# Performance work log

Hardware: AMD Instinct MI355X
Metric: run time of the kernel (lower is better)

Reference implementation:

```python
import jax, jax.numpy as jnp
import numpy as np

HIDDEN = 256


def _lstm_cell(x, h, c, W_ih, W_hh, b_ih, b_hh):
    # torch.nn.LSTMCell: gates ordered [i, f, g, o], gates = x W_ih^T + h W_hh^T + b_ih + b_hh
    gates = x @ W_ih.T + h @ W_hh.T + (b_ih + b_hh)
    i, f, g, o = jnp.split(gates, 4, axis=-1)
    c_new = jax.nn.sigmoid(f) * c + jax.nn.sigmoid(i) * jnp.tanh(g)
    h_new = jax.nn.sigmoid(o) * jnp.tanh(c_new)
    return h_new, c_new


def setup_inputs() -> dict:
    key = jax.random.key(0)
    ks = jax.random.split(key, 16)
    s = 1.0 / np.sqrt(HIDDEN)  # torch LSTMCell init scale
    inp = {
        "tracks": jax.random.normal(ks[0], (256, 512, 2), dtype=jnp.float32),
        "W_ih0": jax.random.uniform(ks[1], (1024, 2), jnp.float32, -s, s),
        "W_hh0": jax.random.uniform(ks[2], (1024, 256), jnp.float32, -s, s),
        "b_ih0": jax.random.uniform(ks[3], (1024,), jnp.float32, -s, s),
        "b_hh0": jax.random.uniform(ks[4], (1024,), jnp.float32, -s, s),
        "W_ih1": jax.random.uniform(ks[5], (1024, 256), jnp.float32, -s, s),
        "W_hh1": jax.random.uniform(ks[6], (1024, 256), jnp.float32, -s, s),
        "b_ih1": jax.random.uniform(ks[7], (1024,), jnp.float32, -s, s),
        "b_hh1": jax.random.uniform(ks[8], (1024,), jnp.float32, -s, s),
        "W_ih2": jax.random.uniform(ks[9], (1024, 256), jnp.float32, -s, s),
        "W_hh2": jax.random.uniform(ks[10], (1024, 256), jnp.float32, -s, s),
        "b_ih2": jax.random.uniform(ks[11], (1024,), jnp.float32, -s, s),
        "b_hh2": jax.random.uniform(ks[12], (1024,), jnp.float32, -s, s),
        "W_pred": jax.random.uniform(ks[13], (2, 256), jnp.float32, -s, s),
        "b_pred": jax.random.uniform(ks[14], (2,), jnp.float32, -s, s),
    }
    return inp


def reference(tracks, W_ih0, W_hh0, b_ih0, b_hh0, W_ih1, W_hh1, b_ih1, b_hh1,
              W_ih2, W_hh2, b_ih2, b_hh2, W_pred, b_pred):
    B = tracks.shape[0]
    layers = [(W_ih0, W_hh0, b_ih0, b_hh0),
              (W_ih1, W_hh1, b_ih1, b_hh1),
              (W_ih2, W_hh2, b_ih2, b_hh2)]
    zeros = jnp.zeros((B, HIDDEN), dtype=tracks.dtype)
    init_carry = tuple((zeros, zeros) for _ in layers)

    def step(carry, x_t):
        new_carry = []
        h = x_t
        for (hc, params) in zip(carry, layers):
            h, c = _lstm_cell(h, hc[0], hc[1], *params)
            new_carry.append((h, c))
        return tuple(new_carry), None

    xs = jnp.swapaxes(tracks, 0, 1)  # [T, B, 2]
    final_carry, _ = jax.lax.scan(step, init_carry, xs)
    h = final_carry[-1][0]  # last layer's final hidden state
    h = jax.nn.elu(h)
    return h @ W_pred.T + b_pred
```

## Files before the change

### kernel.cpp

```cpp
#include <hip/hip_runtime.h>
#include <math.h>

typedef __attribute__((ext_vector_type(4))) float f32x4;
typedef __attribute__((ext_vector_type(4))) int   i32x4;
typedef __attribute__((ext_vector_type(8))) short bfrag8;

#define WRE_LO_OFF 2621440
#define HB_OFF     5242880
#define FA_OFF     6029312
#define FF_OFF     6078464
#define WS_END     6127616

#define WROW 264
#define SMEM_BYTES (4 * 64 * WROW * 2)

__device__ __forceinline__ unsigned short f2bf(float f){
  union { float f; unsigned u; } x; x.f = f;
  unsigned r = x.u + 0x7FFFu + ((x.u >> 16) & 1u);
  return (unsigned short)(r >> 16);
}
__device__ __forceinline__ float bf2f(unsigned short s){
  union { unsigned u; float f; } x; x.u = ((unsigned)s) << 16; return x.f;
}
__device__ __forceinline__ float sigf(float x){
  return 1.0f / (1.0f + __expf(-x));
}
__device__ __forceinline__ float tanh_fast(float x){
  x = fminf(fmaxf(x, -15.0f), 15.0f);
  float e = __expf(2.0f * x);
  return (e - 1.0f) / (e + 1.0f);
}

__device__ __forceinline__ i32x4 llc_load_b128(const void* p){
  i32x4 r;
  asm volatile("global_load_dwordx4 %0, %1, off sc0 sc1"
               : "=v"(r) : "v"(p) : "memory");
  return r;
}
__device__ __forceinline__ void llc_store_b16(void* p, unsigned short v){
  unsigned int vv = v;
  asm volatile("global_store_short %0, %1, off sc0 sc1"
               : : "v"(p), "v"(vv) : "memory");
}
__device__ __forceinline__ void llc_store_u32(void* p, unsigned v){
  asm volatile("global_store_dword %0, %1, off sc0 sc1"
               : : "v"(p), "v"(v) : "memory");
}
__device__ __forceinline__ unsigned poll_llc(const unsigned int* p){
  unsigned r;
  asm volatile("global_load_dword %0, %1, off sc0 sc1\n\ts_waitcnt vmcnt(0)"
               : "=v"(r) : "v"(p) : "memory");
  return r;
}
__device__ __forceinline__ void wait_vm0(){
  asm volatile("s_waitcnt vmcnt(0)" ::: "memory");
}

__global__ void init_reorder(const float* __restrict__ hh0, const float* __restrict__ ih1,
                             const float* __restrict__ hh1, const float* __restrict__ ih2,
                             const float* __restrict__ hh2,
                             unsigned short* __restrict__ wre_hi,
                             unsigned short* __restrict__ wre_lo){
  int e = blockIdx.x * 256 + threadIdx.x;
  int mat = e >> 18;
  int d   = (e >> 8) & 1023;
  int k   = e & 255;
  int nt = d >> 6, g = (d >> 4) & 3, n = d & 15;
  int src_row = g*256 + nt*16 + n;
  const float* W = (mat==0) ? hh0 : (mat==1) ? ih1 : (mat==2) ? hh1 : (mat==3) ? ih2 : hh2;
  float v = W[src_row*256 + k];
  unsigned short hi = f2bf(v);
  float lo = v - bf2f(hi);
  wre_hi[e] = hi;
  wre_lo[e] = f2bf(lo);
}

__global__ void init_zero(uint4* __restrict__ p, int n16){
  int i = blockIdx.x * 256 + threadIdx.x;
  if (i < n16) p[i] = make_uint4(0u,0u,0u,0u);
}

__global__ void lstm_coop(
    const float* __restrict__ tracks,
    const float* __restrict__ wih0,
    const float* __restrict__ bih0, const float* __restrict__ bhh0,
    const float* __restrict__ bih1, const float* __restrict__ bhh1,
    const float* __restrict__ bih2, const float* __restrict__ bhh2,
    const unsigned short* __restrict__ wre_hi, const unsigned short* __restrict__ wre_lo,
    char* __restrict__ wsb)
{
  extern __shared__ __align__(16) unsigned short smem[];

  const int tid  = threadIdx.x;
  const int l    = blockIdx.x >> 6;
  const int r6   = blockIdx.x & 63;
  const int nt   = r6 & 15, bt = r6 >> 4;
  const int b0   = bt * 64, n0 = nt * 16;
  const int w    = tid >> 6, lane = tid & 63;
  const int m    = lane & 15, q = lane >> 4;

  unsigned short* hb = (unsigned short*)(wsb + HB_OFF);

  unsigned* FAb = (unsigned*)(wsb + FA_OFF) + bt*(3*16*64);
  unsigned* FFb = (unsigned*)(wsb + FF_OFF) + bt*(3*16*64);
  unsigned* myA = FAb + (l*16 + nt)*64;
  unsigned* myF = FFb + (l*16 + nt)*64;
  const unsigned* pollp = nullptr;
  if (tid < 16)                                pollp = FFb + (l*16 + tid)*64;
  else if (tid < 32 && l >= 1)                 pollp = FFb + ((l-1)*16 + (tid-16))*64;
  else if (tid >= 32 && tid < 48 && l <= 1)    pollp = FAb + ((l+1)*16 + (tid-32))*64;

  const int nmats = (l == 0) ? 1 : 2;
  const int gmat0 = (l == 0) ? 0 : (l == 1 ? 1 : 3);
  for (int mi = 0; mi < nmats; ++mi){
    const unsigned short* sh = wre_hi + (gmat0 + mi)*262144 + nt*16384;
    const unsigned short* sl = wre_lo + (gmat0 + mi)*262144 + nt*16384;
    unsigned short* dh = smem + (mi*2 + 0)*64*WROW;
    unsigned short* dl = smem + (mi*2 + 1)*64*WROW;
    for (int c = tid; c < 2048; c += 256){
      int r = c >> 5, off = (c & 31) * 8;
      *(uint4*)(dh + r*WROW + off) = *(const uint4*)(sh + r*256 + off);
      *(uint4*)(dl + r*WROW + off) = *(const uint4*)(sl + r*256 + off);
    }
  }
  __syncthreads();

  const float* bihL = (l==0) ? bih0 : (l==1) ? bih1 : bih2;
  const float* bhhL = (l==0) ? bhh0 : (l==1) ? bhh1 : bhh2;
  float bsum[4], wx[4][2];
  #pragma unroll
  for (int g = 0; g < 4; ++g){
    int row = g*256 + n0 + m;
    bsum[g] = bihL[row] + bhhL[row];
    wx[g][0] = wih0[row*2 + 0];
    wx[g][1] = wih0[row*2 + 1];
  }
  float cst[4] = {0.f, 0.f, 0.f, 0.f};
  const int arow = b0 + 16*w + m;
  const int woff = m*WROW + q*8;

  for (int s = 0; s < 514; ++s){
    const int t = s - l;
    const bool active = (t >= 0) && (t < 512);

    float xv0[4], xv1[4];
    if (l == 0 && active){
      #pragma unroll
      for (int r = 0; r < 4; ++r){
        const float* px = tracks + (b0 + 16*w + q*4 + r)*1024 + t*2;
        xv0[r] = px[0]; xv1[r] = px[1];
      }
    }

    if (s > 0){
      if (tid < 64 && pollp != nullptr){
        const unsigned tgt = (unsigned)s;
        int guard = 0;
        while (poll_llc(pollp) < tgt){
          __builtin_amdgcn_s_sleep(1);
          if (++guard > 20000) break;
        }
      }
      __syncthreads();
    }

    i32x4 ar_raw[8], ai_raw[8];
    int pt = 0;
    if (active){
      pt = t & 1;
      const int pp = pt ^ 1;
      const unsigned short* prec = hb + ((pp*3 + l)*256 + arow)*256 + q*8;
      #pragma unroll
      for (int ks = 0; ks < 8; ++ks)
        ar_raw[ks] = llc_load_b128(prec + ks*32);
      if (l >= 1){
        const unsigned short* pin = hb + ((pt*3 + (l-1))*256 + arow)*256 + q*8;
        #pragma unroll
        for (int ks = 0; ks < 8; ++ks)
          ai_raw[ks] = llc_load_b128(pin + ks*32);
      }
      wait_vm0();
      __builtin_amdgcn_sched_barrier(0);
    }
    __syncthreads();
    if (tid == 0) llc_store_u32(myA, (unsigned)(s + 1));

    if (active){
      f32x4 acc[4];
      #pragma unroll
      for (int g = 0; g < 4; ++g) acc[g] = (f32x4){0.f,0.f,0.f,0.f};

      {
        const unsigned short* bh = smem + ((l==0?0:2) + 0)*64*WROW + woff;
        const unsigned short* bl = smem + ((l==0?0:2) + 1)*64*WROW + woff;
        #pragma unroll
        for (int ks = 0; ks < 8; ++ks){
          bfrag8 a = __builtin_bit_cast(bfrag8, ar_raw[ks]);
          #pragma unroll
          for (int g = 0; g < 4; ++g){
            bfrag8 fh = *(const bfrag8*)(bh + g*16*WROW + ks*32);
            bfrag8 fl = *(const bfrag8*)(bl + g*16*WROW + ks*32);
            acc[g] = __builtin_amdgcn_mfma_f32_16x16x32_bf16(a, fh, acc[g], 0, 0, 0);
            acc[g] = __builtin_amdgcn_mfma_f32_16x16x32_bf16(a, fl, acc[g], 0, 0, 0);
          }
        }
      }
      if (l >= 1){
        const unsigned short* bh = smem + 0*64*WROW + woff;
        const unsigned short* bl = smem + 1*64*WROW + woff;
        #pragma unroll
        for (int ks = 0; ks < 8; ++ks){
          bfrag8 a = __builtin_bit_cast(bfrag8, ai_raw[ks]);
          #pragma unroll
          for (int g = 0; g < 4; ++g){
            bfrag8 fh = *(const bfrag8*)(bh + g*16*WROW + ks*32);
            bfrag8 fl = *(const bfrag8*)(bl + g*16*WROW + ks*32);
            acc[g] = __builtin_amdgcn_mfma_f32_16x16x32_bf16(a, fh, acc[g], 0, 0, 0);
            acc[g] = __builtin_amdgcn_mfma_f32_16x16x32_bf16(a, fl, acc[g], 0, 0, 0);
          }
        }
      }

      unsigned short* hout = hb + ((pt*3 + l)*256 + 0)*256;
      #pragma unroll
      for (int r = 0; r < 4; ++r){
        float xi = 0.f, xf = 0.f, xg = 0.f, xo = 0.f;
        if (l == 0){
          xi = xv0[r]*wx[0][0] + xv1[r]*wx[0][1];
          xf = xv0[r]*wx[1][0] + xv1[r]*wx[1][1];
          xg = xv0[r]*wx[2][0] + xv1[r]*wx[2][1];
          xo = xv0[r]*wx[3][0] + xv1[r]*wx[3][1];
        }
        float gi = acc[0][r] + bsum[0] + xi;
        float gf = acc[1][r] + bsum[1] + xf;
        float gg = acc[2][r] + bsum[2] + xg;
        float go = acc[3][r] + bsum[3] + xo;
        float iv = sigf(gi);
        float fv = sigf(gf);
        float gv = tanh_fast(gg);
        float ov = sigf(go);
        cst[r] = fv * cst[r] + iv * gv;
        float hv = ov * tanh_fast(cst[r]);
        llc_store_b16(&hout[(b0 + 16*w + q*4 + r)*256 + n0 + m], f2bf(hv));
      }
    }

    wait_vm0();
    __builtin_amdgcn_sched_barrier(0);
    __syncthreads();
    if (tid == 0) llc_store_u32(myF, (unsigned)(s + 1));
  }
}

__global__ void head_kernel(const unsigned short* __restrict__ hb,
                            const float* __restrict__ wpred,
                            const float* __restrict__ bpred,
                            float* __restrict__ out){
  const int b = blockIdx.x;
  const int k = threadIdx.x;
  const int idx = (5*256 + b)*256 + k;
  float h = bf2f(hb[idx]);
  float e = (h > 0.f) ? h : expm1f(h);
  float v0 = e * wpred[k];
  float v1 = e * wpred[256 + k];
  #pragma unroll
  for (int off = 32; off > 0; off >>= 1){
    v0 += __shfl_down(v0, off, 64);
    v1 += __shfl_down(v1, off, 64);
  }
  __shared__ float r0[4], r1[4];
  int wv = threadIdx.x >> 6, ln = threadIdx.x & 63;
  if (ln == 0){ r0[wv] = v0; r1[wv] = v1; }
  __syncthreads();
  if (threadIdx.x == 0){
    out[b*2 + 0] = r0[0] + r0[1] + r0[2] + r0[3] + bpred[0];
    out[b*2 + 1] = r1[0] + r1[1] + r1[2] + r1[3] + bpred[1];
  }
}

extern "C" void kernel_launch(void* const* d_in, const int* in_sizes, int n_in,
                              void* d_out, int out_size, void* d_ws, size_t ws_size,
                              hipStream_t stream) {
  const float* tracks = (const float*)d_in[0];
  const float* wih0   = (const float*)d_in[1];
  const float* whh0   = (const float*)d_in[2];
  const float* bih0   = (const float*)d_in[3];
  const float* bhh0   = (const float*)d_in[4];
  const float* wih1   = (const float*)d_in[5];
  const float* whh1   = (const float*)d_in[6];
  const float* bih1   = (const float*)d_in[7];
  const float* bhh1   = (const float*)d_in[8];
  const float* wih2   = (const float*)d_in[9];
  const float* whh2   = (const float*)d_in[10];
  const float* bih2   = (const float*)d_in[11];
  const float* bhh2   = (const float*)d_in[12];
  const float* wpred  = (const float*)d_in[13];
  const float* bpred  = (const float*)d_in[14];
  float* out = (float*)d_out;

  char* wsb = (char*)d_ws;
  unsigned short* wre_hi = (unsigned short*)(wsb);
  unsigned short* wre_lo = (unsigned short*)(wsb + WRE_LO_OFF);
  const unsigned short* hb = (const unsigned short*)(wsb + HB_OFF);

  (void)hipFuncSetAttribute((const void*)lstm_coop,
                            hipFuncAttributeMaxDynamicSharedMemorySize, SMEM_BYTES);

  init_reorder<<<5120, 256, 0, stream>>>(whh0, wih1, whh1, wih2, whh2, wre_hi, wre_lo);
  init_zero<<<216, 256, 0, stream>>>((uint4*)(wsb + HB_OFF), 55296);

  void* args[11];
  args[0]  = (void*)&tracks;
  args[1]  = (void*)&wih0;
  args[2]  = (void*)&bih0;
  args[3]  = (void*)&bhh0;
  args[4]  = (void*)&bih1;
  args[5]  = (void*)&bhh1;
  args[6]  = (void*)&bih2;
  args[7]  = (void*)&bhh2;
  args[8]  = (void*)&wre_hi;
  args[9]  = (void*)&wre_lo;
  args[10] = (void*)&wsb;
  hipLaunchCooperativeKernel((const void*)lstm_coop, dim3(192), dim3(256), args,
                             SMEM_BYTES, stream);

  head_kernel<<<256, 256, 0, stream>>>(hb, wpred, bpred, out);
}
```

Before: 4.038 ms.

## Replace lockstep wavefront sync with per-layer ring buffers and decoupled flags

Swaps the global lockstep schedule, where every layer advanced together on one step counter with a double-buffered hidden state and an extra 'consumed' flag per step, for per-layer ring buffers of depth 4 (2 for the last layer). Each block now waits only on its own layer's previous step, the lower layer's current step, and the upper layer lagging by at most three steps. This drops the mid-step barrier and consumed-flag store and lets layers run ahead of one another. It relies on the ring depth and flag targets being correct, and a mistake would give silent data races.

Result: faster. 3.693 ms (-8.5%).

```diff
diff --git a/kernel.cpp b/kernel.cpp
--- a/kernel.cpp
+++ b/kernel.cpp
@@ -6,10 +6,11 @@
 typedef __attribute__((ext_vector_type(8))) short bfrag8;
 
 #define WRE_LO_OFF 2621440
-#define HB_OFF     5242880
-#define FA_OFF     6029312
-#define FF_OFF     6078464
-#define WS_END     6127616
+#define RING0_OFF  5242880
+#define RING1_OFF  5767168
+#define RING2_OFF  6291456
+#define FLG_OFF    6553600
+#define WS_END     6602752
 
 #define WROW 264
 #define SMEM_BYTES (4 * 64 * WROW * 2)
@@ -99,16 +100,19 @@
   const int w    = tid >> 6, lane = tid & 63;
   const int m    = lane & 15, q = lane >> 4;
 
-  unsigned short* hb = (unsigned short*)(wsb + HB_OFF);
-
-  unsigned* FAb = (unsigned*)(wsb + FA_OFF) + bt*(3*16*64);
-  unsigned* FFb = (unsigned*)(wsb + FF_OFF) + bt*(3*16*64);
-  unsigned* myA = FAb + (l*16 + nt)*64;
-  unsigned* myF = FFb + (l*16 + nt)*64;
-  const unsigned* pollp = nullptr;
-  if (tid < 16)                                pollp = FFb + (l*16 + tid)*64;
-  else if (tid < 32 && l >= 1)                 pollp = FFb + ((l-1)*16 + (tid-16))*64;
-  else if (tid >= 32 && tid < 48 && l <= 1)    pollp = FAb + ((l+1)*16 + (tid-32))*64;
+  const int Dm   = (l == 2) ? 1 : 3;
+  unsigned short* ring_own =
+      (unsigned short*)(wsb + ((l==0) ? RING0_OFF : (l==1) ? RING1_OFF : RING2_OFF))
+      + bt * ((l==2) ? 2 : 4) * 16384;
+  unsigned short* ring_low = (l == 0) ? nullptr :
+      (unsigned short*)(wsb + ((l==1) ? RING0_OFF : RING1_OFF)) + bt * 4 * 16384;
+
+  unsigned* FL  = (unsigned*)(wsb + FLG_OFF);
+  unsigned* myF = FL + ((l*4 + bt)*16 + nt)*64;
+  const unsigned* pollp = nullptr; int pcls = 0;
+  if (tid < 16){                         pollp = FL + ((l*4 + bt)*16 + tid)*64;       pcls = 1; }
+  else if (tid < 32 && l >= 1){          pollp = FL + (((l-1)*4 + bt)*16 + (tid-16))*64; pcls = 2; }
+  else if (tid >= 32 && tid < 48 && l <= 1){ pollp = FL + (((l+1)*4 + bt)*16 + (tid-32))*64; pcls = 3; }
 
   const int nmats = (l == 0) ? 1 : 2;
   const int gmat0 = (l == 0) ? 0 : (l == 1 ? 1 : 3);
@@ -136,15 +140,12 @@
     wx[g][1] = wih0[row*2 + 1];
   }
   float cst[4] = {0.f, 0.f, 0.f, 0.f};
-  const int arow = b0 + 16*w + m;
+  const int lrow = 16*w + m;
   const int woff = m*WROW + q*8;
 
-  for (int s = 0; s < 514; ++s){
-    const int t = s - l;
-    const bool active = (t >= 0) && (t < 512);
-
+  for (int t = 0; t < 512; ++t){
     float xv0[4], xv1[4];
-    if (l == 0 && active){
+    if (l == 0){
       #pragma unroll
       for (int r = 0; r < 4; ++r){
         const float* px = tracks + (b0 + 16*w + q*4 + r)*1024 + t*2;
@@ -152,9 +153,12 @@
       }
     }
 
-    if (s > 0){
-      if (tid < 64 && pollp != nullptr){
-        const unsigned tgt = (unsigned)s;
+    {
+      unsigned tgt = 0;
+      if      (pcls == 1) tgt = (unsigned)t;
+      else if (pcls == 2) tgt = (unsigned)(t + 1);
+      else if (pcls == 3) tgt = (t >= 4) ? (unsigned)(t - 3) : 0u;
+      if (tgt){
         int guard = 0;
         while (poll_llc(pollp) < tgt){
           __builtin_amdgcn_s_sleep(1);
@@ -165,101 +169,96 @@
     }
 
     i32x4 ar_raw[8], ai_raw[8];
-    int pt = 0;
-    if (active){
-      pt = t & 1;
-      const int pp = pt ^ 1;
-      const unsigned short* prec = hb + ((pp*3 + l)*256 + arow)*256 + q*8;
+    {
+      const unsigned short* prec = ring_own + ((t-1) & Dm)*16384 + lrow*256 + q*8;
+      if (t == 0) prec = ring_own + Dm*16384 + lrow*256 + q*8;
       #pragma unroll
       for (int ks = 0; ks < 8; ++ks)
         ar_raw[ks] = llc_load_b128(prec + ks*32);
       if (l >= 1){
-        const unsigned short* pin = hb + ((pt*3 + (l-1))*256 + arow)*256 + q*8;
+        const unsigned short* pin = ring_low + (t & 3)*16384 + lrow*256 + q*8;
         #pragma unroll
         for (int ks = 0; ks < 8; ++ks)
           ai_raw[ks] = llc_load_b128(pin + ks*32);
       }
-      wait_vm0();
-      __builtin_amdgcn_sched_barrier(0);
-    }
-    __syncthreads();
-    if (tid == 0) llc_store_u32(myA, (unsigned)(s + 1));
-
-    if (active){
-      f32x4 acc[4];
+    }
+    wait_vm0();
+    __builtin_amdgcn_sched_barrier(0);
+
+    f32x4 acc[4];
+    #pragma unroll
+    for (int g = 0; g < 4; ++g) acc[g] = (f32x4){0.f,0.f,0.f,0.f};
+
+    {
+      const unsigned short* bh = smem + ((l==0?0:2) + 0)*64*WROW + woff;
+      const unsigned short* bl = smem + ((l==0?0:2) + 1)*64*WROW + woff;
       #pragma unroll
-      for (int g = 0; g < 4; ++g) acc[g] = (f32x4){0.f,0.f,0.f,0.f};
-
-      {
-        const unsigned short* bh = smem + ((l==0?0:2) + 0)*64*WROW + woff;
-        const unsigned short* bl = smem + ((l==0?0:2) + 1)*64*WROW + woff;
+      for (int ks = 0; ks < 8; ++ks){
+        bfrag8 a = __builtin_bit_cast(bfrag8, ar_raw[ks]);
         #pragma unroll
-        for (int ks = 0; ks < 8; ++ks){
-          bfrag8 a = __builtin_bit_cast(bfrag8, ar_raw[ks]);
-          #pragma unroll
-          for (int g = 0; g < 4; ++g){
-            bfrag8 fh = *(const bfrag8*)(bh + g*16*WROW + ks*32);
-            bfrag8 fl = *(const bfrag8*)(bl + g*16*WROW + ks*32);
-            acc[g] = __builtin_amdgcn_mfma_f32_16x16x32_bf16(a, fh, acc[g], 0, 0, 0);
-            acc[g] = __builtin_amdgcn_mfma_f32_16x16x32_bf16(a, fl, acc[g], 0, 0, 0);
-          }
+        for (int g = 0; g < 4; ++g){
+          bfrag8 fh = *(const bfrag8*)(bh + g*16*WROW + ks*32);
+          bfrag8 fl = *(const bfrag8*)(bl + g*16*WROW + ks*32);
+          acc[g] = __builtin_amdgcn_mfma_f32_16x16x32_bf16(a, fh, acc[g], 0, 0, 0);
+          acc[g] = __builtin_amdgcn_mfma_f32_16x16x32_bf16(a, fl, acc[g], 0, 0, 0);
         }
       }
-      if (l >= 1){
-        const unsigned short* bh = smem + 0*64*WROW + woff;
-        const unsigned short* bl = smem + 1*64*WROW + woff;
+    }
+    if (l >= 1){
+      const unsigned short* bh = smem + 0*64*WROW + woff;
+      const unsigned short* bl = smem + 1*64*WROW + woff;
+      #pragma unroll
+      for (int ks = 0; ks < 8; ++ks){
+        bfrag8 a = __builtin_bit_cast(bfrag8, ai_raw[ks]);
         #pragma unroll
-        for (int ks = 0; ks < 8; ++ks){
-          bfrag8 a = __builtin_bit_cast(bfrag8, ai_raw[ks]);
-          #pragma unroll
-          for (int g = 0; g < 4; ++g){
-            bfrag8 fh = *(const bfrag8*)(bh + g*16*WROW + ks*32);
-            bfrag8 fl = *(const bfrag8*)(bl + g*16*WROW + ks*32);
-            acc[g] = __builtin_amdgcn_mfma_f32_16x16x32_bf16(a, fh, acc[g], 0, 0, 0);
-            acc[g] = __builtin_amdgcn_mfma_f32_16x16x32_bf16(a, fl, acc[g], 0, 0, 0);
-          }
+        for (int g = 0; g < 4; ++g){
+          bfrag8 fh = *(const bfrag8*)(bh + g*16*WROW + ks*32);
+          bfrag8 fl = *(const bfrag8*)(bl + g*16*WROW + ks*32);
+          acc[g] = __builtin_amdgcn_mfma_f32_16x16x32_bf16(a, fh, acc[g], 0, 0, 0);
+          acc[g] = __builtin_amdgcn_mfma_f32_16x16x32_bf16(a, fl, acc[g], 0, 0, 0);
         }
       }
-
-      unsigned short* hout = hb + ((pt*3 + l)*256 + 0)*256;
-      #pragma unroll
-      for (int r = 0; r < 4; ++r){
-        float xi = 0.f, xf = 0.f, xg = 0.f, xo = 0.f;
-        if (l == 0){
-          xi = xv0[r]*wx[0][0] + xv1[r]*wx[0][1];
-          xf = xv0[r]*wx[1][0] + xv1[r]*wx[1][1];
-          xg = xv0[r]*wx[2][0] + xv1[r]*wx[2][1];
-          xo = xv0[r]*wx[3][0] + xv1[r]*wx[3][1];
-        }
-        float gi = acc[0][r] + bsum[0] + xi;
-        float gf = acc[1][r] + bsum[1] + xf;
-        float gg = acc[2][r] + bsum[2] + xg;
-        float go = acc[3][r] + bsum[3] + xo;
-        float iv = sigf(gi);
-        float fv = sigf(gf);
-        float gv = tanh_fast(gg);
-        float ov = sigf(go);
-        cst[r] = fv * cst[r] + iv * gv;
-        float hv = ov * tanh_fast(cst[r]);
-        llc_store_b16(&hout[(b0 + 16*w + q*4 + r)*256 + n0 + m], f2bf(hv));
-      }
+    }
+
+    unsigned short* hout = ring_own + (t & Dm)*16384;
+    #pragma unroll
+    for (int r = 0; r < 4; ++r){
+      float xi = 0.f, xf = 0.f, xg = 0.f, xo = 0.f;
+      if (l == 0){
+        xi = xv0[r]*wx[0][0] + xv1[r]*wx[0][1];
+        xf = xv0[r]*wx[1][0] + xv1[r]*wx[1][1];
+        xg = xv0[r]*wx[2][0] + xv1[r]*wx[2][1];
+        xo = xv0[r]*wx[3][0] + xv1[r]*wx[3][1];
+      }
+      float gi = acc[0][r] + bsum[0] + xi;
+      float gf = acc[1][r] + bsum[1] + xf;
+      float gg = acc[2][r] + bsum[2] + xg;
+      float go = acc[3][r] + bsum[3] + xo;
+      float iv = sigf(gi);
+      float fv = sigf(gf);
+      float gv = tanh_fast(gg);
+      float ov = sigf(go);
+      cst[r] = fv * cst[r] + iv * gv;
+      float hv = ov * tanh_fast(cst[r]);
+      llc_store_b16(&hout[(16*w + q*4 + r)*256 + n0 + m], f2bf(hv));
     }
 
     wait_vm0();
     __builtin_amdgcn_sched_barrier(0);
     __syncthreads();
-    if (tid == 0) llc_store_u32(myF, (unsigned)(s + 1));
-  }
-}
-
-__global__ void head_kernel(const unsigned short* __restrict__ hb,
+    if (tid == 0) llc_store_u32(myF, (unsigned)(t + 1));
+  }
+}
+
+__global__ void head_kernel(const char* __restrict__ wsb,
                             const float* __restrict__ wpred,
                             const float* __restrict__ bpred,
                             float* __restrict__ out){
   const int b = blockIdx.x;
   const int k = threadIdx.x;
-  const int idx = (5*256 + b)*256 + k;
-  float h = bf2f(hb[idx]);
+  const int bt = b >> 6, row = b & 63;
+  const unsigned short* ring2 = (const unsigned short*)(wsb + RING2_OFF);
+  float h = bf2f(ring2[(bt*2 + 1)*16384 + row*256 + k]);
   float e = (h > 0.f) ? h : expm1f(h);
   float v0 = e * wpred[k];
   float v1 = e * wpred[256 + k];
@@ -301,13 +300,12 @@
   char* wsb = (char*)d_ws;
   unsigned short* wre_hi = (unsigned short*)(wsb);
   unsigned short* wre_lo = (unsigned short*)(wsb + WRE_LO_OFF);
-  const unsigned short* hb = (const unsigned short*)(wsb + HB_OFF);
 
   (void)hipFuncSetAttribute((const void*)lstm_coop,
                             hipFuncAttributeMaxDynamicSharedMemorySize, SMEM_BYTES);
 
   init_reorder<<<5120, 256, 0, stream>>>(whh0, wih1, whh1, wih2, whh2, wre_hi, wre_lo);
-  init_zero<<<216, 256, 0, stream>>>((uint4*)(wsb + HB_OFF), 55296);
+  init_zero<<<332, 256, 0, stream>>>((uint4*)(wsb + RING0_OFF), 84992);
 
   void* args[11];
   args[0]  = (void*)&tracks;
@@ -324,5 +322,5 @@
   hipLaunchCooperativeKernel((const void*)lstm_coop, dim3(192), dim3(256), args,
                              SMEM_BYTES, stream);
 
-  head_kernel<<<256, 256, 0, stream>>>(hb, wpred, bpred, out);
-}
+  head_kernel<<<256, 256, 0, stream>>>(wsb, wpred, bpred, out);
+}
```
